# Performance work log

Measured on AMD Instinct MI355X. Metric: run time of the kernel, lower is better.

## Reference

```python
import jax, jax.numpy as jnp
import numpy as np

B, S = 4, 2048          # batch, seq tokens
D_IN, D_HID = 1280, 2048  # from CAMERAMOE emb_size / d_inner
E, K = 8, 2             # num_experts, top_k
LN_EPS = 1e-6


def setup_inputs() -> dict:
    key = jax.random.key(0)
    ks = jax.random.split(key, 8)
    rn = lambda k, shp, sc=1.0: jax.random.normal(k, shp, dtype=jnp.float32) * sc
    return {
        "x": rn(ks[0], (B, S, D_IN)),
        "noise": rn(ks[1], (B, S, E)),          # the randn_like draw, made explicit
        "wr": rn(ks[2], (D_IN, E), 0.02), "br": jnp.zeros((E,), jnp.float32),
        "wn": rn(ks[3], (D_IN, E), 0.02), "bn": jnp.zeros((E,), jnp.float32),
        "w1": rn(ks[4], (E, D_IN, D_HID), 0.02), "b1": jnp.zeros((E, D_HID), jnp.float32),
        "w2": rn(ks[5], (E, D_HID, D_IN), 0.02), "b2": jnp.zeros((E, D_IN), jnp.float32),
        "gamma": jnp.ones((E, D_IN), jnp.float32), "beta": jnp.zeros((E, D_IN), jnp.float32),
    }


def reference(x, noise, wr, br, wn, bn, w1, b1, w2, b2, gamma, beta):
    # --- NoisyTopkRouter ---
    logits = x @ wr + br                                  # [B,S,E]
    noise_logits = x @ wn + bn                            # [B,S,E]
    noisy = logits + noise * jax.nn.softplus(noise_logits)
    _, idx = jax.lax.top_k(noisy, K)                      # [B,S,K]
    sel = jax.nn.one_hot(idx, E, dtype=bool).any(axis=-2) # [B,S,E] selected-expert mask
    sparse_logits = jnp.where(sel, noisy, -jnp.inf)       # scatter of top-k logits into -inf
    gates = jax.nn.softmax(sparse_logits, axis=-1)        # zeros for non-selected experts

    # --- SparseMoE combine (gate-weighted sum over experts; gate==0 masks out
    # non-selected tokens, matching the torch masked gather/scatter-add math) ---
    h = jax.nn.relu(jnp.einsum('bsd,edh->ebsh', x, w1) + b1[:, None, None, :])
    y = jnp.einsum('ebsh,ehd->ebsd', h, w2) + b2[:, None, None, :]
    y = y + x                                             # residual (broadcast over E)
    mu = y.mean(axis=-1, keepdims=True)
    var = y.var(axis=-1, keepdims=True)
    y = (y - mu) * jax.lax.rsqrt(var + LN_EPS)
    y = y * gamma[:, None, None, :] + beta[:, None, None, :]
    return jnp.einsum('ebsd,bse->bsd', y, gates)          # [B,S,D_IN]
```

## Files before the change

### kernel.cpp

```cpp
#include <hip/hip_runtime.h>
#include <stdint.h>

typedef unsigned short u16;
typedef __attribute__((ext_vector_type(8))) short short8;
typedef __attribute__((ext_vector_type(4))) float f32x4;
typedef __attribute__((ext_vector_type(4))) float float4v;
typedef __attribute__((ext_vector_type(4))) unsigned short us4;
typedef __attribute__((ext_vector_type(8))) unsigned short us8;

#define TOK   8192
#define DIN   1280
#define DHID  2048
#define NEXP  8
#define RCAP  17408
#define MT128 136

#define TRBLK1 5120
#define TRBLK2 5120
#define RTRBLKS 1024

__device__ __forceinline__ float bf2f(u16 u) {
  union { unsigned int i; float f; } v; v.i = ((unsigned int)u) << 16; return v.f;
}
__device__ __forceinline__ u16 f2bf(float f) {
  union { float f; unsigned int i; } v; v.f = f;
  unsigned int x = v.i;
  return (u16)((x + 0x7fffu + ((x >> 16) & 1u)) >> 16);
}

__device__ __forceinline__ void gload16(const u16* g, void* lds) {
  __builtin_amdgcn_global_load_lds(
      (const __attribute__((address_space(1))) unsigned int*)g,
      (__attribute__((address_space(3))) unsigned int*)lds, 16, 0, 0);
}

__global__ __launch_bounds__(256) void pre_k(
    const float* __restrict__ w1, u16* __restrict__ W1t,
    const float* __restrict__ w2, u16* __restrict__ W2t,
    const float* __restrict__ x, const float* __restrict__ noise,
    const float* __restrict__ wr, const float* __restrict__ br,
    const float* __restrict__ wn, const float* __restrict__ bn,
    int* __restrict__ topk_e, float* __restrict__ topk_g)
{
  __shared__ u16 ldsT[64 * 72];
  int id = blockIdx.x;
  int tid = threadIdx.x;
  int w = tid >> 6, lane = tid & 63;

  if (id < TRBLK1 + TRBLK2) {
    const float* in; u16* outp; int RK, CN, rb, cb;
    if (id < TRBLK1) {
      int e = id / 640, r = id % 640;
      RK = DIN; CN = DHID;
      rb = (r >> 5) * 64; cb = (r & 31) * 64;
      in = w1 + (size_t)e * RK * CN; outp = W1t + (size_t)e * RK * CN;
    } else {
      int id2 = id - TRBLK1;
      int e = id2 / 640, r = id2 % 640;
      RK = DHID; CN = DIN;
      rb = (r / 20) * 64; cb = (r % 20) * 64;
      in = w2 + (size_t)e * RK * CN; outp = W2t + (size_t)e * RK * CN;
    }
    {
      const float* src = in + (size_t)(rb + lane) * CN + cb + w * 16;
      u16 val[16];
      #pragma unroll
      for (int k = 0; k < 4; k++) {
        float4v v = *(const float4v*)(src + k * 4);
        #pragma unroll
        for (int j = 0; j < 4; j++) val[k * 4 + j] = f2bf(v[j]);
      }
      #pragma unroll
      for (int j = 0; j < 16; j++)
        ldsT[(w * 16 + j) * 72 + lane] = val[j];
    }
    __syncthreads();
    {
      int oc = tid >> 2, rch = (tid & 3) * 16;
      const u16* s = &ldsT[oc * 72 + rch];
      u16* d = outp + (size_t)(cb + oc) * RK + rb + rch;
      *(us8*)(d)     = *(const us8*)(s);
      *(us8*)(d + 8) = *(const us8*)(s + 8);
    }
    return;
  }

  int rid = id - (TRBLK1 + TRBLK2);
  int t0 = rid * 8 + w * 2;
  const float4v* xA = (const float4v*)(x + (size_t)t0 * DIN);
  const float4v* xB = (const float4v*)(x + (size_t)(t0 + 1) * DIN);
  float accA[16], accB[16];
  #pragma unroll
  for (int k = 0; k < 16; k++) { accA[k] = 0.f; accB[k] = 0.f; }

  #pragma unroll
  for (int i = 0; i < 5; i++) {
    int d4 = i * 64 + lane;
    float4v va = xA[d4];
    float4v vb = xB[d4];
    #pragma unroll
    for (int j = 0; j < 4; j++) {
      int d = d4 * 4 + j;
      const float4v* wrp = (const float4v*)(wr + (size_t)d * 8);
      const float4v* wnp = (const float4v*)(wn + (size_t)d * 8);
      float4v r0 = wrp[0], r1 = wrp[1], n0 = wnp[0], n1 = wnp[1];
      float a = va[j], b = vb[j];
      #pragma unroll
      for (int e = 0; e < 4; e++) {
        accA[e]    += a * r0[e]; accA[e+4]  += a * r1[e];
        accA[e+8]  += a * n0[e]; accA[e+12] += a * n1[e];
        accB[e]    += b * r0[e]; accB[e+4]  += b * r1[e];
        accB[e+8]  += b * n0[e]; accB[e+12] += b * n1[e];
      }
    }
  }
  #pragma unroll
  for (int k = 0; k < 16; k++) {
    float v = accA[k];
    for (int off = 32; off; off >>= 1) v += __shfl_xor(v, off);
    accA[k] = v;
    float u = accB[k];
    for (int off = 32; off; off >>= 1) u += __shfl_xor(u, off);
    accB[k] = u;
  }
  if (lane == 0) {
    #pragma unroll
    for (int tt = 0; tt < 2; tt++) {
      int t = t0 + tt;
      float noisy[8];
      #pragma unroll
      for (int e = 0; e < 8; e++) {
        float lg = (tt ? accB[e] : accA[e]) + br[e];
        float nl = (tt ? accB[e+8] : accA[e+8]) + bn[e];
        float sp = (nl > 0.f) ? nl + log1pf(expf(-nl)) : log1pf(expf(nl));
        noisy[e] = lg + noise[(size_t)t * 8 + e] * sp;
      }
      int e0 = 0; float v0 = noisy[0];
      #pragma unroll
      for (int e = 1; e < 8; e++) if (noisy[e] > v0) { v0 = noisy[e]; e0 = e; }
      int e1 = -1; float v1 = -1e30f;
      #pragma unroll
      for (int e = 0; e < 8; e++) if (e != e0 && noisy[e] > v1) { v1 = noisy[e]; e1 = e; }
      float g0 = 1.f / (1.f + expf(v1 - v0));
      topk_e[2*t] = e0; topk_e[2*t+1] = e1;
      topk_g[2*t] = g0; topk_g[2*t+1] = 1.f - g0;
    }
  }
}

__global__ __launch_bounds__(1024) void scan_k(
    const int* __restrict__ topk_e, int* __restrict__ rowmap, int* __restrict__ aoffs)
{
  __shared__ int cnt[1024][8];
  __shared__ int tot[8];
  __shared__ int base[8];
  int tid = threadIdx.x;
  int ebuf[16];
  #pragma unroll
  for (int j = 0; j < 16; j++) ebuf[j] = topk_e[tid * 16 + j];
  int c0=0,c1=0,c2=0,c3=0,c4=0,c5=0,c6=0,c7=0;
  #pragma unroll
  for (int j = 0; j < 16; j++) {
    int e = ebuf[j];
    c0 += (e==0); c1 += (e==1); c2 += (e==2); c3 += (e==3);
    c4 += (e==4); c5 += (e==5); c6 += (e==6); c7 += (e==7);
  }
  cnt[tid][0]=c0; cnt[tid][1]=c1; cnt[tid][2]=c2; cnt[tid][3]=c3;
  cnt[tid][4]=c4; cnt[tid][5]=c5; cnt[tid][6]=c6; cnt[tid][7]=c7;
  __syncthreads();

  int w = tid >> 6, lane = tid & 63;
  if (w < 8) {
    int e = w;
    int s[16]; int run = 0;
    #pragma unroll
    for (int j = 0; j < 16; j++) { s[j] = run; run += cnt[lane*16+j][e]; }
    int inc = run;
    for (int off = 1; off < 64; off <<= 1) {
      int v = __shfl_up(inc, off);
      if (lane >= off) inc += v;
    }
    int lane_excl = inc - run;
    #pragma unroll
    for (int j = 0; j < 16; j++) cnt[lane*16+j][e] = lane_excl + s[j];
    if (lane == 63) tot[e] = inc;
  }
  __syncthreads();
  if (tid == 0) {
    int a = 0;
    for (int e = 0; e < 8; e++) { base[e] = a; aoffs[e] = a; a += (tot[e] + 127) & ~127; }
    aoffs[8] = a;
  }
  __syncthreads();
  int o0 = base[0]+cnt[tid][0], o1 = base[1]+cnt[tid][1], o2 = base[2]+cnt[tid][2],
      o3 = base[3]+cnt[tid][3], o4 = base[4]+cnt[tid][4], o5 = base[5]+cnt[tid][5],
      o6 = base[6]+cnt[tid][6], o7 = base[7]+cnt[tid][7];
  #pragma unroll
  for (int j = 0; j < 16; j++) {
    int e = ebuf[j];
    int row = o0;
    row = (e==1) ? o1 : row; row = (e==2) ? o2 : row; row = (e==3) ? o3 : row;
    row = (e==4) ? o4 : row; row = (e==5) ? o5 : row; row = (e==6) ? o6 : row;
    row = (e==7) ? o7 : row;
    o0 += (e==0); o1 += (e==1); o2 += (e==2); o3 += (e==3);
    o4 += (e==4); o5 += (e==5); o6 += (e==6); o7 += (e==7);
    rowmap[tid * 16 + j] = row;
  }
}

__global__ __launch_bounds__(256) void gather_k(
    const float* __restrict__ x, const int* __restrict__ rowmap,
    u16* __restrict__ Xe)
{
  int w = threadIdx.x >> 6, lane = threadIdx.x & 63;
  int t = blockIdx.x * 4 + w;
  int r0 = rowmap[2*t], r1 = rowmap[2*t+1];
  const float4v* xs = (const float4v*)(x + (size_t)t * DIN);
  us4* d0 = (us4*)(Xe + (size_t)r0 * DIN);
  us4* d1 = (us4*)(Xe + (size_t)r1 * DIN);
  #pragma unroll
  for (int i = 0; i < DIN / 4 / 64; i++) {
    int q = i * 64 + lane;
    float4v v = xs[q];
    us4 o;
    #pragma unroll
    for (int j = 0; j < 4; j++) o[j] = f2bf(v[j]);
    d0[q] = o;
    d1[q] = o;
  }
}

__global__ __launch_bounds__(256, 2) void gemm128_k(
    const u16* __restrict__ A, const u16* __restrict__ Bt,
    const float* __restrict__ bias, u16* __restrict__ Out,
    const int* __restrict__ aoffs, int K, int N, int relu)
{
  extern __shared__ u16 sm[];

  int nwgx = gridDim.x;
  int id = blockIdx.y * nwgx + blockIdx.x;
  int per = (nwgx * gridDim.y) >> 3;
  int sid = (id & 7) * per + (id >> 3);
  int bx = sid % nwgx, by = sid / nwgx;

  int row0 = by * 128;
  if (row0 >= aoffs[NEXP]) return;
  int e = 0;
  #pragma unroll
  for (int i = 0; i < NEXP; i++) if (row0 >= aoffs[i + 1]) e = i + 1;
  int ncol0 = bx * 128;
  const u16* Ab = A + (size_t)row0 * K;
  const u16* Bb = Bt + ((size_t)e * N + ncol0) * K;

  int tid = threadIdx.x, w = tid >> 6, lane = tid & 63;
  int wr = w >> 1, wc = w & 1;
  int l15 = lane & 15, l4 = lane >> 4;
  int xorv = (l15 & 7) << 3;

  int srow[4], skc[4];
  #pragma unroll
  for (int q = 0; q < 4; q++) {
    int cd = q * 256 + tid;
    int cs = cd ^ ((cd >> 3) & 7);
    srow[q] = cs >> 3;
    skc[q]  = (cs & 7) * 8;
  }
  int ldsw = w * 1024;

  f32x4 acc[4][4];
  #pragma unroll
  for (int m = 0; m < 4; m++)
    #pragma unroll
    for (int n = 0; n < 4; n++) acc[m][n] = (f32x4){0.f, 0.f, 0.f, 0.f};

  short8 a[4][2], b0[2][2], b1[2][2];

#define STAGE_A(T, BUF) do {                                                  \
    char* d_ = (char*)sm + (BUF) * 32768;                                     \
    int ko_ = (T) * 64;                                                       \
    _Pragma("unroll")                                                         \
    for (int q = 0; q < 4; q++)                                               \
      gload16(Ab + (size_t)srow[q] * K + ko_ + skc[q], d_ + q*4096 + ldsw);   \
  } while (0)
#define STAGE_B(T, BUF) do {                                                  \
    char* d_ = (char*)sm + (BUF) * 32768 + 16384;                             \
    int ko_ = (T) * 64;                                                       \
    _Pragma("unroll")                                                         \
    for (int q = 0; q < 4; q++)                                               \
      gload16(Bb + (size_t)srow[q] * K + ko_ + skc[q], d_ + q*4096 + ldsw);   \
  } while (0)
#define RD_A() do {                                                           \
    _Pragma("unroll")                                                         \
    for (int m = 0; m < 4; m++)                                               \
      _Pragma("unroll")                                                       \
      for (int ks = 0; ks < 2; ks++) {                                        \
        int r_ = wr*64 + m*16 + l15;                                          \
        a[m][ks] = *(const short8*)&smA[(r_*64 + ks*32 + l4*8) ^ xorv];       \
      }                                                                       \
  } while (0)
#define RD_B(DST, NH) do {                                                    \
    _Pragma("unroll")                                                         \
    for (int n = 0; n < 2; n++)                                               \
      _Pragma("unroll")                                                       \
      for (int ks = 0; ks < 2; ks++) {                                        \
        int r_ = wc*64 + (NH)*32 + n*16 + l15;                                \
        DST[n][ks] = *(const short8*)&smB[(r_*64 + ks*32 + l4*8) ^ xorv];     \
      }                                                                       \
  } while (0)
#define MFMA16(NH, BB) do {                                                   \
    _Pragma("unroll")                                                         \
    for (int m = 0; m < 4; m++)                                               \
      _Pragma("unroll")                                                       \
      for (int n = 0; n < 2; n++)                                             \
        _Pragma("unroll")                                                     \
        for (int ks = 0; ks < 2; ks++)                                        \
          acc[m][(NH)*2+n] = __builtin_amdgcn_mfma_f32_16x16x32_bf16(         \
              a[m][ks], BB[n][ks], acc[m][(NH)*2+n], 0, 0, 0);                \
  } while (0)
#define BAR __builtin_amdgcn_s_barrier()

  int NT = K >> 6;
  STAGE_A(0, 0);
  STAGE_B(0, 0);
  STAGE_A(1, 1);
  STAGE_B(1, 1);
  asm volatile("s_waitcnt vmcnt(8)" ::: "memory");
  BAR;

  for (int t = 0; t < NT; ++t) {
    int buf = t & 1;
    const u16* smA = sm + buf * 16384;
    const u16* smB = smA + 8192;
    RD_A();
    RD_B(b0, 0);
    RD_B(b1, 1);
    asm volatile("s_waitcnt lgkmcnt(0)" ::: "memory");
    BAR;
    if (t + 2 < NT) {
      STAGE_A(t + 2, buf);
      STAGE_B(t + 2, buf);
    }
    __builtin_amdgcn_s_setprio(1);
    MFMA16(0, b0);
    MFMA16(1, b1);
    __builtin_amdgcn_s_setprio(0);
    if (t + 2 < NT) {
      asm volatile("s_waitcnt vmcnt(8)" ::: "memory");
    } else if (t + 1 < NT) {
      asm volatile("s_waitcnt vmcnt(0)" ::: "memory");
    }
    BAR;
  }
#undef STAGE_A
#undef STAGE_B
#undef RD_A
#undef RD_B
#undef MFMA16
#undef BAR

  #pragma unroll
  for (int in = 0; in < 4; in++) {
    int c = ncol0 + wc * 64 + in * 16 + l15;
    float bv = bias[(size_t)e * N + c];
    #pragma unroll
    for (int im = 0; im < 4; im++) {
      int rb = row0 + wr * 64 + im * 16 + l4 * 4;
      #pragma unroll
      for (int j = 0; j < 4; j++) {
        float v = acc[im][in][j] + bv;
        if (relu) v = fmaxf(v, 0.f);
        Out[(size_t)(rb + j) * N + c] = f2bf(v);
      }
    }
  }
}

__global__ __launch_bounds__(256) void ln_k(
    const float* __restrict__ x, const u16* __restrict__ Y,
    const int* __restrict__ rowmap, const int* __restrict__ topk_e,
    const float* __restrict__ topk_g, const float* __restrict__ gamma,
    const float* __restrict__ beta, float* __restrict__ out)
{
  __shared__ float red[4][4];
  int t = blockIdx.x, tid = threadIdx.x;
  int r0 = rowmap[2*t], r1 = rowmap[2*t+1];
  int e0 = topk_e[2*t], e1 = topk_e[2*t+1];
  float g0 = topk_g[2*t], g1 = topk_g[2*t+1];
  const float* xt = x + (size_t)t * DIN;
  const u16* y0p = Y + (size_t)r0 * DIN;
  const u16* y1p = Y + (size_t)r1 * DIN;
  float v0[5], v1[5];
  float s0 = 0.f, q0 = 0.f, s1 = 0.f, q1 = 0.f;
  #pragma unroll
  for (int i = 0; i < 5; i++) {
    int d = i * 256 + tid;
    float xv = xt[d];
    float a = xv + bf2f(y0p[d]);
    float b = xv + bf2f(y1p[d]);
    v0[i] = a; v1[i] = b;
    s0 += a; q0 += a * a; s1 += b; q1 += b * b;
  }
  for (int off = 32; off; off >>= 1) {
    s0 += __shfl_xor(s0, off); q0 += __shfl_xor(q0, off);
    s1 += __shfl_xor(s1, off); q1 += __shfl_xor(q1, off);
  }
  int w = tid >> 6, lane = tid & 63;
  if (lane == 0) { red[w][0] = s0; red[w][1] = q0; red[w][2] = s1; red[w][3] = q1; }
  __syncthreads();
  s0 = red[0][0] + red[1][0] + red[2][0] + red[3][0];
  q0 = red[0][1] + red[1][1] + red[2][1] + red[3][1];
  s1 = red[0][2] + red[1][2] + red[2][2] + red[3][2];
  q1 = red[0][3] + red[1][3] + red[2][3] + red[3][3];
  const float inv = 1.f / DIN;
  float mu0 = s0 * inv, mu1 = s1 * inv;
  float rs0 = rsqrtf(fmaxf(q0 * inv - mu0 * mu0, 0.f) + 1e-6f);
  float rs1 = rsqrtf(fmaxf(q1 * inv - mu1 * mu1, 0.f) + 1e-6f);
  const float* ga0 = gamma + (size_t)e0 * DIN;
  const float* be0 = beta  + (size_t)e0 * DIN;
  const float* ga1 = gamma + (size_t)e1 * DIN;
  const float* be1 = beta  + (size_t)e1 * DIN;
  #pragma unroll
  for (int i = 0; i < 5; i++) {
    int d = i * 256 + tid;
    float n0 = (v0[i] - mu0) * rs0 * ga0[d] + be0[d];
    float n1 = (v1[i] - mu1) * rs1 * ga1[d] + be1[d];
    out[(size_t)t * DIN + d] = g0 * n0 + g1 * n1;
  }
}

extern "C" void kernel_launch(void* const* d_in, const int* in_sizes, int n_in,
                              void* d_out, int out_size, void* d_ws, size_t ws_size,
                              hipStream_t stream)
{
  const float* x     = (const float*)d_in[0];
  const float* noise = (const float*)d_in[1];
  const float* wr    = (const float*)d_in[2];
  const float* br    = (const float*)d_in[3];
  const float* wn    = (const float*)d_in[4];
  const float* bn    = (const float*)d_in[5];
  const float* w1    = (const float*)d_in[6];
  const float* b1    = (const float*)d_in[7];
  const float* w2    = (const float*)d_in[8];
  const float* b2    = (const float*)d_in[9];
  const float* gamma = (const float*)d_in[10];
  const float* beta  = (const float*)d_in[11];
  float* out = (float*)d_out;
  char* ws = (char*)d_ws;

  int*   aoffs   = (int*)(ws + 128);
  int*   rowmap  = (int*)(ws + 4096);
  int*   topk_e  = (int*)(ws + 4096 + 65536);
  float* topk_g  = (float*)(ws + 4096 + 2 * 65536);

  const size_t XE_OFF   = (size_t)1 << 20;
  const size_t XE_BYTES = (size_t)RCAP * DIN * 2;
  const size_t H_BYTES  = (size_t)RCAP * DHID * 2;
  const size_t WT_BYTES = (size_t)NEXP * DHID * DIN * 2;
  u16* Xe  = (u16*)(ws + XE_OFF);
  u16* Hb  = (u16*)(ws + XE_OFF + XE_BYTES);
  u16* Yb  = Xe;
  u16* W1t = (u16*)(ws + XE_OFF + XE_BYTES + H_BYTES);
  u16* W2t = (u16*)(ws + XE_OFF + XE_BYTES + H_BYTES + WT_BYTES);

  pre_k<<<TRBLK1 + TRBLK2 + RTRBLKS, 256, 0, stream>>>(
      w1, W1t, w2, W2t, x, noise, wr, br, wn, bn, topk_e, topk_g);
  scan_k<<<1, 1024, 0, stream>>>(topk_e, rowmap, aoffs);
  gather_k<<<TOK/4, 256, 0, stream>>>(x, rowmap, Xe);
  gemm128_k<<<dim3(DHID/128, MT128), 256, 65536, stream>>>(Xe, W1t, b1, Hb, aoffs, DIN, DHID, 1);
  gemm128_k<<<dim3(DIN/128, MT128), 256, 65536, stream>>>(Hb, W2t, b2, Yb, aoffs, DHID, DIN, 0);
  ln_k<<<TOK, 256, 0, stream>>>(x, Yb, rowmap, topk_e, topk_g, gamma, beta, out);
}
```

Measured before the change: 362.1 us.

## Split router from weight transpose and remap router lanes to halve reductions

Splits the fused pre-kernel into a separate router kernel and a weight-transpose kernel. The transpose is launched after the scan, and the router is reworked so each lane pair covers one input dimension with the two halves of the 8 experts. This cuts per-lane accumulators from 32 to 16 and shortens the shuffle reduction. The router's x loads become scalar strided reads instead of float4, and an extra kernel launch is added.

```diff
diff --git a/kernel.cpp b/kernel.cpp
--- a/kernel.cpp
+++ b/kernel.cpp
@@ -17,7 +17,6 @@
 
 #define TRBLK1 5120
 #define TRBLK2 5120
-#define RTRBLKS 1024
 
 __device__ __forceinline__ float bf2f(u16 u) {
   union { unsigned int i; float f; } v; v.i = ((unsigned int)u) << 16; return v.f;
@@ -34,94 +33,96 @@
       (__attribute__((address_space(3))) unsigned int*)lds, 16, 0, 0);
 }
 
-__global__ __launch_bounds__(256) void pre_k(
+__global__ __launch_bounds__(256) void tr_k(
     const float* __restrict__ w1, u16* __restrict__ W1t,
-    const float* __restrict__ w2, u16* __restrict__ W2t,
+    const float* __restrict__ w2, u16* __restrict__ W2t)
+{
+  __shared__ u16 ldsT[64 * 72];
+  int id = blockIdx.x;
+  int tid = threadIdx.x;
+  int w = tid >> 6, lane = tid & 63;
+
+  const float* in; u16* outp; int RK, CN, rb, cb;
+  if (id < TRBLK1) {
+    int e = id / 640, r = id % 640;
+    RK = DIN; CN = DHID;
+    rb = (r >> 5) * 64; cb = (r & 31) * 64;
+    in = w1 + (size_t)e * RK * CN; outp = W1t + (size_t)e * RK * CN;
+  } else {
+    int id2 = id - TRBLK1;
+    int e = id2 / 640, r = id2 % 640;
+    RK = DHID; CN = DIN;
+    rb = (r / 20) * 64; cb = (r % 20) * 64;
+    in = w2 + (size_t)e * RK * CN; outp = W2t + (size_t)e * RK * CN;
+  }
+  {
+    const float* src = in + (size_t)(rb + lane) * CN + cb + w * 16;
+    u16 val[16];
+    #pragma unroll
+    for (int k = 0; k < 4; k++) {
+      float4v v = *(const float4v*)(src + k * 4);
+      #pragma unroll
+      for (int j = 0; j < 4; j++) val[k * 4 + j] = f2bf(v[j]);
+    }
+    #pragma unroll
+    for (int j = 0; j < 16; j++)
+      ldsT[(w * 16 + j) * 72 + lane] = val[j];
+  }
+  __syncthreads();
+  {
+    int oc = tid >> 2, rch = (tid & 3) * 16;
+    const u16* s = &ldsT[oc * 72 + rch];
+    u16* d = outp + (size_t)(cb + oc) * RK + rb + rch;
+    *(us8*)(d)     = *(const us8*)(s);
+    *(us8*)(d + 8) = *(const us8*)(s + 8);
+  }
+}
+
+__global__ __launch_bounds__(256) void router_k(
     const float* __restrict__ x, const float* __restrict__ noise,
     const float* __restrict__ wr, const float* __restrict__ br,
     const float* __restrict__ wn, const float* __restrict__ bn,
     int* __restrict__ topk_e, float* __restrict__ topk_g)
 {
-  __shared__ u16 ldsT[64 * 72];
-  int id = blockIdx.x;
-  int tid = threadIdx.x;
-  int w = tid >> 6, lane = tid & 63;
-
-  if (id < TRBLK1 + TRBLK2) {
-    const float* in; u16* outp; int RK, CN, rb, cb;
-    if (id < TRBLK1) {
-      int e = id / 640, r = id % 640;
-      RK = DIN; CN = DHID;
-      rb = (r >> 5) * 64; cb = (r & 31) * 64;
-      in = w1 + (size_t)e * RK * CN; outp = W1t + (size_t)e * RK * CN;
-    } else {
-      int id2 = id - TRBLK1;
-      int e = id2 / 640, r = id2 % 640;
-      RK = DHID; CN = DIN;
-      rb = (r / 20) * 64; cb = (r % 20) * 64;
-      in = w2 + (size_t)e * RK * CN; outp = W2t + (size_t)e * RK * CN;
-    }
-    {
-      const float* src = in + (size_t)(rb + lane) * CN + cb + w * 16;
-      u16 val[16];
-      #pragma unroll
-      for (int k = 0; k < 4; k++) {
-        float4v v = *(const float4v*)(src + k * 4);
-        #pragma unroll
-        for (int j = 0; j < 4; j++) val[k * 4 + j] = f2bf(v[j]);
-      }
-      #pragma unroll
-      for (int j = 0; j < 16; j++)
-        ldsT[(w * 16 + j) * 72 + lane] = val[j];
-    }
-    __syncthreads();
-    {
-      int oc = tid >> 2, rch = (tid & 3) * 16;
-      const u16* s = &ldsT[oc * 72 + rch];
-      u16* d = outp + (size_t)(cb + oc) * RK + rb + rch;
-      *(us8*)(d)     = *(const us8*)(s);
-      *(us8*)(d + 8) = *(const us8*)(s + 8);
-    }
-    return;
-  }
-
-  int rid = id - (TRBLK1 + TRBLK2);
-  int t0 = rid * 8 + w * 2;
-  const float4v* xA = (const float4v*)(x + (size_t)t0 * DIN);
-  const float4v* xB = (const float4v*)(x + (size_t)(t0 + 1) * DIN);
-  float accA[16], accB[16];
-  #pragma unroll
-  for (int k = 0; k < 16; k++) { accA[k] = 0.f; accB[k] = 0.f; }
-
-  #pragma unroll
-  for (int i = 0; i < 5; i++) {
-    int d4 = i * 64 + lane;
-    float4v va = xA[d4];
-    float4v vb = xB[d4];
+  int w = threadIdx.x >> 6, lane = threadIdx.x & 63;
+  int t0 = blockIdx.x * 8 + w * 2;
+  int h = lane & 1, dl = lane >> 1;
+  const float* xA = x + (size_t)t0 * DIN;
+  const float* xB = xA + DIN;
+
+  float ra[4], na[4], rb2[4], nb2[4];
+  #pragma unroll
+  for (int j = 0; j < 4; j++) { ra[j] = 0.f; na[j] = 0.f; rb2[j] = 0.f; nb2[j] = 0.f; }
+
+  #pragma unroll 4
+  for (int d0 = 0; d0 < DIN; d0 += 32) {
+    int d = d0 + dl;
+    float4v wrv = *(const float4v*)(wr + (size_t)d * 8 + h * 4);
+    float4v wnv = *(const float4v*)(wn + (size_t)d * 8 + h * 4);
+    float xa = xA[d], xb = xB[d];
     #pragma unroll
     for (int j = 0; j < 4; j++) {
-      int d = d4 * 4 + j;
-      const float4v* wrp = (const float4v*)(wr + (size_t)d * 8);
-      const float4v* wnp = (const float4v*)(wn + (size_t)d * 8);
-      float4v r0 = wrp[0], r1 = wrp[1], n0 = wnp[0], n1 = wnp[1];
-      float a = va[j], b = vb[j];
-      #pragma unroll
-      for (int e = 0; e < 4; e++) {
-        accA[e]    += a * r0[e]; accA[e+4]  += a * r1[e];
-        accA[e+8]  += a * n0[e]; accA[e+12] += a * n1[e];
-        accB[e]    += b * r0[e]; accB[e+4]  += b * r1[e];
-        accB[e+8]  += b * n0[e]; accB[e+12] += b * n1[e];
-      }
-    }
-  }
-  #pragma unroll
-  for (int k = 0; k < 16; k++) {
-    float v = accA[k];
-    for (int off = 32; off; off >>= 1) v += __shfl_xor(v, off);
-    accA[k] = v;
-    float u = accB[k];
-    for (int off = 32; off; off >>= 1) u += __shfl_xor(u, off);
-    accB[k] = u;
+      ra[j]  += xa * wrv[j]; na[j]  += xa * wnv[j];
+      rb2[j] += xb * wrv[j]; nb2[j] += xb * wnv[j];
+    }
+  }
+  #pragma unroll
+  for (int off = 2; off < 64; off <<= 1) {
+    #pragma unroll
+    for (int j = 0; j < 4; j++) {
+      ra[j]  += __shfl_xor(ra[j],  off);
+      na[j]  += __shfl_xor(na[j],  off);
+      rb2[j] += __shfl_xor(rb2[j], off);
+      nb2[j] += __shfl_xor(nb2[j], off);
+    }
+  }
+  float raO[4], naO[4], rbO[4], nbO[4];
+  #pragma unroll
+  for (int j = 0; j < 4; j++) {
+    raO[j] = __shfl_xor(ra[j], 1);
+    naO[j] = __shfl_xor(na[j], 1);
+    rbO[j] = __shfl_xor(rb2[j], 1);
+    nbO[j] = __shfl_xor(nb2[j], 1);
   }
   if (lane == 0) {
     #pragma unroll
@@ -129,11 +130,15 @@
       int t = t0 + tt;
       float noisy[8];
       #pragma unroll
-      for (int e = 0; e < 8; e++) {
-        float lg = (tt ? accB[e] : accA[e]) + br[e];
-        float nl = (tt ? accB[e+8] : accA[e+8]) + bn[e];
-        float sp = (nl > 0.f) ? nl + log1pf(expf(-nl)) : log1pf(expf(nl));
-        noisy[e] = lg + noise[(size_t)t * 8 + e] * sp;
+      for (int j = 0; j < 4; j++) {
+        float lg0 = (tt ? rb2[j] : ra[j]) + br[j];
+        float nl0 = (tt ? nb2[j] : na[j]) + bn[j];
+        float lg1 = (tt ? rbO[j] : raO[j]) + br[4 + j];
+        float nl1 = (tt ? nbO[j] : naO[j]) + bn[4 + j];
+        float sp0 = (nl0 > 0.f) ? nl0 + log1pf(expf(-nl0)) : log1pf(expf(nl0));
+        float sp1 = (nl1 > 0.f) ? nl1 + log1pf(expf(-nl1)) : log1pf(expf(nl1));
+        noisy[j]     = lg0 + noise[(size_t)t * 8 + j] * sp0;
+        noisy[4 + j] = lg1 + noise[(size_t)t * 8 + 4 + j] * sp1;
       }
       int e0 = 0; float v0 = noisy[0];
       #pragma unroll
@@ -462,9 +467,9 @@
   u16* W1t = (u16*)(ws + XE_OFF + XE_BYTES + H_BYTES);
   u16* W2t = (u16*)(ws + XE_OFF + XE_BYTES + H_BYTES + WT_BYTES);
 
-  pre_k<<<TRBLK1 + TRBLK2 + RTRBLKS, 256, 0, stream>>>(
-      w1, W1t, w2, W2t, x, noise, wr, br, wn, bn, topk_e, topk_g);
+  router_k<<<TOK/8, 256, 0, stream>>>(x, noise, wr, br, wn, bn, topk_e, topk_g);
   scan_k<<<1, 1024, 0, stream>>>(topk_e, rowmap, aoffs);
+  tr_k<<<TRBLK1 + TRBLK2, 256, 0, stream>>>(w1, W1t, w2, W2t);
   gather_k<<<TOK/4, 256, 0, stream>>>(x, rowmap, Xe);
   gemm128_k<<<dim3(DHID/128, MT128), 256, 65536, stream>>>(Xe, W1t, b1, Hb, aoffs, DIN, DHID, 1);
   gemm128_k<<<dim3(DIN/128, MT128), 256, 65536, stream>>>(Hb, W2t, b2, Yb, aoffs, DHID, DIN, 0);
```

New measurement: 341.5 us. -5.7%, faster.
